# Optimization experiments

Hardware: AMD Instinct MI355X
Metric: run time of the kernel (lower is better)

The kernel has to match this reference:

```python
import jax, jax.numpy as jnp
import numpy as np

B, C, IN = 8, 1024, 256
OUT, H, NS, SD = 256, 4, 5, 64
DK = OUT // H


def setup_inputs() -> dict:
    key = jax.random.key(0)
    ks = jax.random.split(key, 16)
    s = lambda k, *shape: jax.random.normal(k, shape, dtype=jnp.float32) * 0.05
    return {
        "x": jax.random.normal(ks[0], (B, C, IN), dtype=jnp.float32),
        "A_prior": jax.random.uniform(ks[1], (C, C), dtype=jnp.float32),
        # lin_project
        "Wp": s(ks[2], IN, OUT), "bp": jnp.zeros((OUT,), jnp.float32),
        # stage_mlp: Linear(IN,128) -> ReLU -> Linear(128,NS)
        "Ws1": s(ks[3], IN, 128), "bs1": jnp.zeros((128,), jnp.float32),
        "Ws2": s(ks[4], 128, NS), "bs2": jnp.zeros((NS,), jnp.float32),
        # mlp_c: Linear(NS,SD) -> ReLU -> Linear(SD,SD)
        "Wc1": s(ks[5], NS, SD), "bc1": jnp.zeros((SD,), jnp.float32),
        "Wc2": s(ks[6], SD, SD), "bc2": jnp.zeros((SD,), jnp.float32),
        # att_scorer: Linear(2*DK+SD, 1, bias=False) -> weight vector
        "att_w": s(ks[7], 2 * DK + SD),
        "lam": jnp.ones((H,), jnp.float32),
    }


def reference(x, A_prior, Wp, bp, Ws1, bs1, Ws2, bs2, Wc1, bc1, Wc2, bc2, att_w, lam):
    # projection -> (B, C, H, DK)
    x_proj = (x @ Wp + bp).reshape(B, C, H, DK)
    # stage logits from mean-pooled features
    s_logits = jax.nn.relu(x.mean(axis=1) @ Ws1 + bs1) @ Ws2 + bs2  # (B, NS)
    s_prob = jax.nn.softmax(s_logits, axis=-1)
    c = jax.nn.relu(s_prob @ Wc1 + bc1) @ Wc2 + bc2  # (B, SD)
    # att_scorer is linear over cat([x_src, x_dst, c]); decompose weight to
    # avoid materializing the (B,C,C,H,2*DK+SD) concat tensor.
    w_src, w_dst, w_c = att_w[:DK], att_w[DK:2 * DK], att_w[2 * DK:]
    src_s = jnp.einsum('bjhd,d->bjh', x_proj, w_src)  # x_src[b,i,j] = x_proj[b,j]
    dst_s = jnp.einsum('bihd,d->bih', x_proj, w_dst)  # x_dst[b,i,j] = x_proj[b,i]
    c_s = c @ w_c                                      # (B,)
    e = jax.nn.leaky_relu(
        src_s[:, None, :, :] + dst_s[:, :, None, :] + c_s[:, None, None, None],
        negative_slope=0.2)                            # (B, C, C, H)
    prior = lam[None, None, None, :] * jnp.log(A_prior[None, :, :, None] + 1e-9)
    alpha = jax.nn.softmax(e + prior, axis=2)          # softmax over src j
    out = jnp.einsum('bijh,bjhd->bihd', alpha, x_proj).reshape(B, C, OUT)
    return out, s_logits
```

## Files before the change

### kernel.cpp

```cpp
#include <hip/hip_runtime.h>
#include <hip/hip_fp16.h>

typedef _Float16 f16x8 __attribute__((ext_vector_type(8)));
typedef _Float16 f16x4 __attribute__((ext_vector_type(4)));
typedef float f32x4 __attribute__((ext_vector_type(4)));

#define NB 8
#define NNS 5


__global__ __launch_bounds__(256) void k_pre(const float* __restrict__ Wp,
                                             const float* __restrict__ x,
                                             const float* __restrict__ A,
                                             __half* __restrict__ WpF,
                                             float* __restrict__ xmean,
                                             __half* __restrict__ l2AF) {
  const int t = threadIdx.x;
  const int blk = blockIdx.x;
  if (blk < 256) {
    const int idx = (blk << 8) + t;
    const int u = idx & 7, lane = (idx >> 3) & 63;
    const int kc = (idx >> 9) & 7, nt = (idx >> 12) & 3, nh = idx >> 14;
    const int f = (nh << 6) + (nt << 4) + (lane & 15);
    const int k = (kc << 5) + (((lane >> 4)) << 3) + u;
    WpF[idx] = __float2half(Wp[(k << 8) + f]);
  } else if (blk < 512) {
    const int row0 = (blk - 256) << 5;
    const int b = row0 >> 10;
    float ps = 0.f;
    #pragma unroll 8
    for (int r = 0; r < 32; ++r) ps += x[(size_t)(row0 + r) * 256 + t];
    atomicAdd(&xmean[(b << 8) + t], ps);
  } else {
    const int idx = ((blk - 512) << 8) + t;
    const int u = idx & 7, lane = (idx >> 3) & 63;
    const int jc = (idx >> 9) & 31, it = idx >> 14;
    const int row = (it << 4) + (lane & 15);
    const int j = (jc << 5) + ((lane >> 4) << 3) + u;
    l2AF[idx] = __float2half(__log2f(A[((size_t)row << 10) + j] + 1e-9f));
  }
}

__global__ __launch_bounds__(256, 4) void k_projM(
    const float* __restrict__ x, const __half* __restrict__ WpF,
    const float* __restrict__ bp, const float* __restrict__ att_w,
    __half* __restrict__ xpF, float* __restrict__ srcT,
    float* __restrict__ dstT) {
  __shared__ __align__(16) __half xs[64 * 256];
  const int t = threadIdx.x;
  const int l = t & 63, w = t >> 6;
  const int lm = l & 15, q = l >> 4;
  const int rg = blockIdx.x >> 2, nh = blockIdx.x & 3;
  const int row0 = rg << 6;

  #pragma unroll
  for (int it = 0; it < 16; ++it) {
    const int fi = (it << 8) + t;
    const int row = fi >> 6, c4 = fi & 63;
    const f32x4 v = *(const f32x4*)(x + (size_t)(row0 + row) * 256 + (c4 << 2));
    f16x4 hv;
    #pragma unroll
    for (int u = 0; u < 4; ++u) hv[u] = (_Float16)v[u];
    const int byte = (row << 9) + (c4 << 3);
    *(f16x4*)((char*)xs + (byte ^ ((row & 7) << 4))) = hv;
  }
  __syncthreads();

  const char* ar = (char*)xs + (((w << 4) + lm) << 9);
  const int xa = (lm & 7) << 4;
  const __half* Bw = WpF + (nh << 14) + (l << 3);

  f32x4 acc0 = {0.f, 0.f, 0.f, 0.f}, acc1 = acc0, acc2 = acc0, acc3 = acc0;
  #pragma unroll
  for (int kc = 0; kc < 8; ++kc) {
    const f16x8 af =
        *(const f16x8*)(ar + ((((kc << 5) + (q << 3)) << 1) ^ xa));
    const f16x8 b0 = *(const f16x8*)(Bw + (kc << 9));
    const f16x8 b1 = *(const f16x8*)(Bw + (kc << 9) + 4096);
    const f16x8 b2 = *(const f16x8*)(Bw + (kc << 9) + 8192);
    const f16x8 b3 = *(const f16x8*)(Bw + (kc << 9) + 12288);
    acc0 = __builtin_amdgcn_mfma_f32_16x16x32_f16(af, b0, acc0, 0, 0, 0);
    acc1 = __builtin_amdgcn_mfma_f32_16x16x32_f16(af, b1, acc1, 0, 0, 0);
    acc2 = __builtin_amdgcn_mfma_f32_16x16x32_f16(af, b2, acc2, 0, 0, 0);
    acc3 = __builtin_amdgcn_mfma_f32_16x16x32_f16(af, b3, acc3, 0, 0, 0);
  }

  const int Rw = row0 + (w << 4);
  const int b = Rw >> 10;
  const int il = (Rw & 1023) + (q << 2);
  const int jc = il >> 5, lq = (il >> 3) & 3, u0 = il & 7;
  const int lane_o = (lq << 4) + lm;
  f32x4 accs[4] = {acc0, acc1, acc2, acc3};
  float wsn[4], wdn[4];
  #pragma unroll
  for (int n = 0; n < 4; ++n) {
    const int d = (n << 4) + lm;
    wsn[n] = att_w[d];
    wdn[n] = att_w[64 + d];
  }
  const size_t base = ((((size_t)((b << 2) + nh) << 5) + jc) << 2);
  #pragma unroll
  for (int n = 0; n < 4; ++n) {
    const float bias = bp[(nh << 6) + (n << 4) + lm];
    f16x4 o;
    #pragma unroll
    for (int reg = 0; reg < 4; ++reg) {
      accs[n][reg] += bias;
      o[reg] = (_Float16)accs[n][reg];
    }
    *(f16x4*)(xpF + (((base + n) << 9) + (lane_o << 3) + u0)) = o;
  }
  #pragma unroll
  for (int reg = 0; reg < 4; ++reg) {
    float ss = 0.f, ds = 0.f;
    #pragma unroll
    for (int n = 0; n < 4; ++n) {
      ss = fmaf(accs[n][reg], wsn[n], ss);
      ds = fmaf(accs[n][reg], wdn[n], ds);
    }
    #pragma unroll
    for (int off = 1; off < 16; off <<= 1) {
      ss += __shfl_xor(ss, off);
      ds += __shfl_xor(ds, off);
    }
    if (lm == 0) {
      const int i = il + reg;
      srcT[(((b << 2) + nh) << 10) + i] = ss;
      dstT[(((b << 2) + nh) << 10) + i] = ds;
    }
  }
}

__global__ __launch_bounds__(256) void k_head(
    const float* __restrict__ Ws1, const float* __restrict__ bs1,
    const float* __restrict__ Ws2, const float* __restrict__ bs2,
    const float* __restrict__ Wc1, const float* __restrict__ bc1,
    const float* __restrict__ Wc2, const float* __restrict__ bc2,
    const float* __restrict__ att_w, const float* __restrict__ xmean,
    float* __restrict__ cs_ws, float* __restrict__ out_slogits) {
  __shared__ float xm[256];
  __shared__ float h1p[2][128];
  __shared__ float h1[128];
  __shared__ float sl[NNS];
  __shared__ float sp[NNS];
  __shared__ float cc1[64];
  __shared__ float cvec[64];
  const int b = blockIdx.x, t = threadIdx.x;
  xm[t] = xmean[b * 256 + t] * (1.f / 1024.f);
  __syncthreads();
  {
    const int kh = t >> 7, f = t & 127;
    const float* wcol = Ws1 + (kh << 7) * 128 + f;
    const float* xk = xm + (kh << 7);
    float a = 0.f;
    #pragma unroll 8
    for (int k = 0; k < 128; ++k) a = fmaf(xk[k], wcol[k * 128], a);
    h1p[kh][f] = a;
  }
  __syncthreads();
  if (t < 128) h1[t] = fmaxf(h1p[0][t] + h1p[1][t] + bs1[t], 0.f);
  __syncthreads();
  if (t < NNS) {
    float a = bs2[t];
    #pragma unroll 8
    for (int k = 0; k < 128; ++k) a = fmaf(h1[k], Ws2[k * NNS + t], a);
    sl[t] = a;
    out_slogits[b * NNS + t] = a;
  }
  __syncthreads();
  if (t == 0) {
    float m = sl[0];
    for (int n = 1; n < NNS; ++n) m = fmaxf(m, sl[n]);
    float s = 0.f;
    for (int n = 0; n < NNS; ++n) { sp[n] = expf(sl[n] - m); s += sp[n]; }
    for (int n = 0; n < NNS; ++n) sp[n] /= s;
  }
  __syncthreads();
  if (t < 64) {
    float a = bc1[t];
    #pragma unroll
    for (int n = 0; n < NNS; ++n) a = fmaf(sp[n], Wc1[n * 64 + t], a);
    cc1[t] = fmaxf(a, 0.f);
  }
  __syncthreads();
  if (t < 64) {
    float a = bc2[t];
    #pragma unroll 8
    for (int m = 0; m < 64; ++m) a = fmaf(cc1[m], Wc2[m * 64 + t], a);
    cvec[t] = a;
  }
  __syncthreads();
  if (t < 64) {
    float v = cvec[t] * att_w[128 + t];
    #pragma unroll
    for (int m = 32; m; m >>= 1) v += __shfl_xor(v, m);
    if (t == 0) cs_ws[b] = v;
  }
}

__global__ __launch_bounds__(1024, 8) void k_attn(
    const __half* __restrict__ xpF, const __half* __restrict__ l2AF,
    const float* __restrict__ srcT, const float* __restrict__ dstT,
    const float* __restrict__ cs_ws, const float* __restrict__ lam,
    float* __restrict__ out) {
  __shared__ float red[3][4][4][16][18];
  __shared__ float dsum[4][4][16];
  const int t = threadIdx.x;
  const int l = t & 63, w = t >> 6;
  const int h = w & 3, jq = w >> 2;
  const int lm = l & 15, q = l >> 4;
  const int b = blockIdx.x >> 6;
  const int tile = blockIdx.x & 63;
  const int i0 = tile << 4;

  const float csv = cs_ws[b];
  const float lamln2 = lam[h] * 0.69314718056f;
  const float dstc = dstT[(((b << 2) + h) << 10) + i0 + lm] + csv;

  const __half* Lp =
      l2AF + ((((size_t)(tile << 5) + (jq << 3)) << 6) + l) * 8;
  const float* Sp = srcT + (((b << 2) + h) << 10) + (jq << 8) + (q << 3);
  const __half* Bp =
      xpF + ((((size_t)((b << 2) + h) << 5) + (jq << 3)) << 11) + (l << 3);

  f32x4 acc0 = {0.f, 0.f, 0.f, 0.f}, acc1 = acc0, acc2 = acc0, acc3 = acc0;
  float sum = 0.f;

  #pragma unroll
  for (int kk = 0; kk < 8; ++kk) {
    const f16x8 la = *(const f16x8*)(Lp + (kk << 9));
    const f16x8 bf0 = *(const f16x8*)(Bp + (kk << 11));
    const f16x8 bf1 = *(const f16x8*)(Bp + (kk << 11) + 512);
    const f16x8 bf2 = *(const f16x8*)(Bp + (kk << 11) + 1024);
    const f16x8 bf3 = *(const f16x8*)(Bp + (kk << 11) + 1536);
    const f32x4 s0 = *(const f32x4*)(Sp + (kk << 5));
    const f32x4 s1 = *(const f32x4*)(Sp + (kk << 5) + 4);
    f16x8 af;
    #pragma unroll
    for (int u = 0; u < 4; ++u) {
      float e0 = s0[u] + dstc;
      e0 = fmaxf(e0, 0.2f * e0);
      const float p0 = __expf(fmaf(lamln2, (float)la[u], e0));
      sum += p0;
      af[u] = (_Float16)p0;
      float e1 = s1[u] + dstc;
      e1 = fmaxf(e1, 0.2f * e1);
      const float p1 = __expf(fmaf(lamln2, (float)la[u + 4], e1));
      sum += p1;
      af[u + 4] = (_Float16)p1;
    }
    acc0 = __builtin_amdgcn_mfma_f32_16x16x32_f16(af, bf0, acc0, 0, 0, 0);
    acc1 = __builtin_amdgcn_mfma_f32_16x16x32_f16(af, bf1, acc1, 0, 0, 0);
    acc2 = __builtin_amdgcn_mfma_f32_16x16x32_f16(af, bf2, acc2, 0, 0, 0);
    acc3 = __builtin_amdgcn_mfma_f32_16x16x32_f16(af, bf3, acc3, 0, 0, 0);
  }

  sum += __shfl_xor(sum, 16);
  sum += __shfl_xor(sum, 32);
  if (l < 16) dsum[h][jq][lm] = sum;
  if (jq != 0) {
    #pragma unroll
    for (int reg = 0; reg < 4; ++reg) {
      const int mrow = (q << 2) + reg;
      red[jq - 1][h][0][mrow][lm] = acc0[reg];
      red[jq - 1][h][1][mrow][lm] = acc1[reg];
      red[jq - 1][h][2][mrow][lm] = acc2[reg];
      red[jq - 1][h][3][mrow][lm] = acc3[reg];
    }
  }
  __syncthreads();
  if (jq == 0) {
    float* ob =
        out + (((size_t)((b << 10) + i0)) << 8) + (h << 6) + lm;
    #pragma unroll
    for (int reg = 0; reg < 4; ++reg) {
      const int mrow = (q << 2) + reg;
      const float dv = 1.f / (dsum[h][0][mrow] + dsum[h][1][mrow] +
                              dsum[h][2][mrow] + dsum[h][3][mrow]);
      const float v0 = acc0[reg] + red[0][h][0][mrow][lm] +
                       red[1][h][0][mrow][lm] + red[2][h][0][mrow][lm];
      const float v1 = acc1[reg] + red[0][h][1][mrow][lm] +
                       red[1][h][1][mrow][lm] + red[2][h][1][mrow][lm];
      const float v2 = acc2[reg] + red[0][h][2][mrow][lm] +
                       red[1][h][2][mrow][lm] + red[2][h][2][mrow][lm];
      const float v3 = acc3[reg] + red[0][h][3][mrow][lm] +
                       red[1][h][3][mrow][lm] + red[2][h][3][mrow][lm];
      float* orow = ob + ((size_t)mrow << 8);
      orow[0] = v0 * dv;
      orow[16] = v1 * dv;
      orow[32] = v2 * dv;
      orow[48] = v3 * dv;
    }
  }
}

extern "C" void kernel_launch(void* const* d_in, const int* in_sizes, int n_in,
                              void* d_out, int out_size, void* d_ws,
                              size_t ws_size, hipStream_t stream) {
  const float* x     = (const float*)d_in[0];
  const float* A     = (const float*)d_in[1];
  const float* Wp    = (const float*)d_in[2];
  const float* bp    = (const float*)d_in[3];
  const float* Ws1   = (const float*)d_in[4];
  const float* bs1   = (const float*)d_in[5];
  const float* Ws2   = (const float*)d_in[6];
  const float* bs2   = (const float*)d_in[7];
  const float* Wc1   = (const float*)d_in[8];
  const float* bc1   = (const float*)d_in[9];
  const float* Wc2   = (const float*)d_in[10];
  const float* bc2   = (const float*)d_in[11];
  const float* att_w = (const float*)d_in[12];
  const float* lam   = (const float*)d_in[13];
  float* out = (float*)d_out;
  float* ws  = (float*)d_ws;

  __half* xpF  = (__half*)ws;
  __half* l2AF = (__half*)(ws + 1048576);
  float* srcT  = ws + 1572864;
  float* dstT  = ws + 1605632;
  float* xmean = ws + 1638400;
  float* cs    = ws + 1640448;
  __half* WpF  = (__half*)(ws + 1640456);

  hipMemsetAsync(xmean, 0, 2048 * sizeof(float), stream);

  k_pre<<<dim3(4608), dim3(256), 0, stream>>>(Wp, x, A, WpF, xmean, l2AF);
  k_projM<<<dim3(512), dim3(256), 0, stream>>>(x, WpF, bp, att_w, xpF, srcT,
                                               dstT);
  k_head<<<dim3(NB), dim3(256), 0, stream>>>(Ws1, bs1, Ws2, bs2, Wc1, bc1,
                                             Wc2, bc2, att_w, xmean, cs,
                                             out + NB * 1024 * 256);
  k_attn<<<dim3(512), dim3(1024), 0, stream>>>(xpF, l2AF, srcT, dstT, cs, lam,
                                               out);
}
```

Measured before the change: 130.0 us.

## Fuse x fp16 conversion into pre-pass, halve attention split-K with prefetching

The mean-pooling pre-pass now also converts x to fp16 in MFMA-fragment order, so the projection kernel loads A-fragments straight from global memory without LDS staging. The attention kernel drops from 4 to 2 j-chunks per head (512 threads), with a 16-step loop that prefetches the next iteration's operands, which shrinks the cross-wave LDS reduction. Costs are an extra fp16 workspace buffer with its global write and read, and longer per-wave serial loops with higher register pressure.

```diff
diff --git a/kernel.cpp b/kernel.cpp
--- a/kernel.cpp
+++ b/kernel.cpp
@@ -14,7 +14,9 @@
                                              const float* __restrict__ A,
                                              __half* __restrict__ WpF,
                                              float* __restrict__ xmean,
+                                             __half* __restrict__ xF,
                                              __half* __restrict__ l2AF) {
+  __shared__ __align__(16) float xs[32][260];
   const int t = threadIdx.x;
   const int blk = blockIdx.x;
   if (blk < 256) {
@@ -22,15 +24,40 @@
     const int u = idx & 7, lane = (idx >> 3) & 63;
     const int kc = (idx >> 9) & 7, nt = (idx >> 12) & 3, nh = idx >> 14;
     const int f = (nh << 6) + (nt << 4) + (lane & 15);
-    const int k = (kc << 5) + (((lane >> 4)) << 3) + u;
+    const int k = (kc << 5) + ((lane >> 4) << 3) + u;
     WpF[idx] = __float2half(Wp[(k << 8) + f]);
   } else if (blk < 512) {
     const int row0 = (blk - 256) << 5;
     const int b = row0 >> 10;
+    const int rt0 = row0 >> 4;
     float ps = 0.f;
     #pragma unroll 8
-    for (int r = 0; r < 32; ++r) ps += x[(size_t)(row0 + r) * 256 + t];
+    for (int r = 0; r < 32; ++r) {
+      const float v = x[(size_t)(row0 + r) * 256 + t];
+      xs[r][t] = v;
+      ps += v;
+    }
     atomicAdd(&xmean[(b << 8) + t], ps);
+    __syncthreads();
+    #pragma unroll
+    for (int it = 0; it < 4; ++it) {
+      const int oi = it * 256 + t;
+      const int lane = oi & 63;
+      const int kc = (oi >> 6) & 7;
+      const int rtl = oi >> 9;
+      const int row_l = (rtl << 4) + (lane & 15);
+      const int k0 = (kc << 5) + ((lane >> 4) << 3);
+      const f32x4 va = *(const f32x4*)&xs[row_l][k0];
+      const f32x4 vb = *(const f32x4*)&xs[row_l][k0 + 4];
+      f16x8 hv;
+      #pragma unroll
+      for (int u = 0; u < 4; ++u) {
+        hv[u] = (_Float16)va[u];
+        hv[u + 4] = (_Float16)vb[u];
+      }
+      *(f16x8*)(xF + (((size_t)(rt0 + rtl)) << 12) + (kc << 9) + (lane << 3)) =
+          hv;
+    }
   } else {
     const int idx = ((blk - 512) << 8) + t;
     const int u = idx & 7, lane = (idx >> 3) & 63;
@@ -42,52 +69,39 @@
 }
 
 __global__ __launch_bounds__(256, 4) void k_projM(
-    const float* __restrict__ x, const __half* __restrict__ WpF,
+    const __half* __restrict__ xF, const __half* __restrict__ WpF,
     const float* __restrict__ bp, const float* __restrict__ att_w,
     __half* __restrict__ xpF, float* __restrict__ srcT,
     float* __restrict__ dstT) {
-  __shared__ __align__(16) __half xs[64 * 256];
   const int t = threadIdx.x;
   const int l = t & 63, w = t >> 6;
   const int lm = l & 15, q = l >> 4;
   const int rg = blockIdx.x >> 2, nh = blockIdx.x & 3;
-  const int row0 = rg << 6;
-
-  #pragma unroll
-  for (int it = 0; it < 16; ++it) {
-    const int fi = (it << 8) + t;
-    const int row = fi >> 6, c4 = fi & 63;
-    const f32x4 v = *(const f32x4*)(x + (size_t)(row0 + row) * 256 + (c4 << 2));
-    f16x4 hv;
-    #pragma unroll
-    for (int u = 0; u < 4; ++u) hv[u] = (_Float16)v[u];
-    const int byte = (row << 9) + (c4 << 3);
-    *(f16x4*)((char*)xs + (byte ^ ((row & 7) << 4))) = hv;
-  }
-  __syncthreads();
-
-  const char* ar = (char*)xs + (((w << 4) + lm) << 9);
-  const int xa = (lm & 7) << 4;
+  const int rt = (rg << 2) + w;
+  const int R0 = rt << 4;
+
+  const __half* Ap = xF + (((size_t)rt) << 12) + (l << 3);
   const __half* Bw = WpF + (nh << 14) + (l << 3);
 
+  f16x8 ah[8];
+  #pragma unroll
+  for (int kc = 0; kc < 8; ++kc) ah[kc] = *(const f16x8*)(Ap + (kc << 9));
+
   f32x4 acc0 = {0.f, 0.f, 0.f, 0.f}, acc1 = acc0, acc2 = acc0, acc3 = acc0;
   #pragma unroll
   for (int kc = 0; kc < 8; ++kc) {
-    const f16x8 af =
-        *(const f16x8*)(ar + ((((kc << 5) + (q << 3)) << 1) ^ xa));
     const f16x8 b0 = *(const f16x8*)(Bw + (kc << 9));
     const f16x8 b1 = *(const f16x8*)(Bw + (kc << 9) + 4096);
     const f16x8 b2 = *(const f16x8*)(Bw + (kc << 9) + 8192);
     const f16x8 b3 = *(const f16x8*)(Bw + (kc << 9) + 12288);
-    acc0 = __builtin_amdgcn_mfma_f32_16x16x32_f16(af, b0, acc0, 0, 0, 0);
-    acc1 = __builtin_amdgcn_mfma_f32_16x16x32_f16(af, b1, acc1, 0, 0, 0);
-    acc2 = __builtin_amdgcn_mfma_f32_16x16x32_f16(af, b2, acc2, 0, 0, 0);
-    acc3 = __builtin_amdgcn_mfma_f32_16x16x32_f16(af, b3, acc3, 0, 0, 0);
-  }
-
-  const int Rw = row0 + (w << 4);
-  const int b = Rw >> 10;
-  const int il = (Rw & 1023) + (q << 2);
+    acc0 = __builtin_amdgcn_mfma_f32_16x16x32_f16(ah[kc], b0, acc0, 0, 0, 0);
+    acc1 = __builtin_amdgcn_mfma_f32_16x16x32_f16(ah[kc], b1, acc1, 0, 0, 0);
+    acc2 = __builtin_amdgcn_mfma_f32_16x16x32_f16(ah[kc], b2, acc2, 0, 0, 0);
+    acc3 = __builtin_amdgcn_mfma_f32_16x16x32_f16(ah[kc], b3, acc3, 0, 0, 0);
+  }
+
+  const int b = R0 >> 10;
+  const int il = (R0 & 1023) + (q << 2);
   const int jc = il >> 5, lq = (il >> 3) & 3, u0 = il & 7;
   const int lane_o = (lq << 4) + lm;
   f32x4 accs[4] = {acc0, acc1, acc2, acc3};
@@ -198,16 +212,16 @@
   }
 }
 
-__global__ __launch_bounds__(1024, 8) void k_attn(
+__global__ __launch_bounds__(512, 4) void k_attn(
     const __half* __restrict__ xpF, const __half* __restrict__ l2AF,
     const float* __restrict__ srcT, const float* __restrict__ dstT,
     const float* __restrict__ cs_ws, const float* __restrict__ lam,
     float* __restrict__ out) {
-  __shared__ float red[3][4][4][16][18];
-  __shared__ float dsum[4][4][16];
+  __shared__ float red[4][4][16][18];
+  __shared__ float dsum[4][2][16];
   const int t = threadIdx.x;
   const int l = t & 63, w = t >> 6;
-  const int h = w & 3, jq = w >> 2;
+  const int h = w & 3, jh = w >> 2;
   const int lm = l & 15, q = l >> 4;
   const int b = blockIdx.x >> 6;
   const int tile = blockIdx.x & 63;
@@ -217,24 +231,33 @@
   const float lamln2 = lam[h] * 0.69314718056f;
   const float dstc = dstT[(((b << 2) + h) << 10) + i0 + lm] + csv;
 
-  const __half* Lp =
-      l2AF + ((((size_t)(tile << 5) + (jq << 3)) << 6) + l) * 8;
-  const float* Sp = srcT + (((b << 2) + h) << 10) + (jq << 8) + (q << 3);
+  const __half* Lp = l2AF + (tile << 14) + (jh << 13) + (l << 3);
+  const float* Sp = srcT + (((b << 2) + h) << 10) + (jh << 9) + (q << 3);
   const __half* Bp =
-      xpF + ((((size_t)((b << 2) + h) << 5) + (jq << 3)) << 11) + (l << 3);
+      xpF + (((size_t)((b << 2) + h)) << 16) + (jh << 15) + (l << 3);
 
   f32x4 acc0 = {0.f, 0.f, 0.f, 0.f}, acc1 = acc0, acc2 = acc0, acc3 = acc0;
   float sum = 0.f;
 
-  #pragma unroll
-  for (int kk = 0; kk < 8; ++kk) {
-    const f16x8 la = *(const f16x8*)(Lp + (kk << 9));
-    const f16x8 bf0 = *(const f16x8*)(Bp + (kk << 11));
-    const f16x8 bf1 = *(const f16x8*)(Bp + (kk << 11) + 512);
-    const f16x8 bf2 = *(const f16x8*)(Bp + (kk << 11) + 1024);
-    const f16x8 bf3 = *(const f16x8*)(Bp + (kk << 11) + 1536);
-    const f32x4 s0 = *(const f32x4*)(Sp + (kk << 5));
-    const f32x4 s1 = *(const f32x4*)(Sp + (kk << 5) + 4);
+  f16x8 la = *(const f16x8*)Lp;
+  f32x4 s0 = *(const f32x4*)Sp;
+  f32x4 s1 = *(const f32x4*)(Sp + 4);
+  f16x8 bf0 = *(const f16x8*)Bp;
+  f16x8 bf1 = *(const f16x8*)(Bp + 512);
+  f16x8 bf2 = *(const f16x8*)(Bp + 1024);
+  f16x8 bf3 = *(const f16x8*)(Bp + 1536);
+
+  #pragma unroll 4
+  for (int kk = 0; kk < 16; ++kk) {
+    const int nk = (kk < 15) ? kk + 1 : kk;
+    const f16x8 la_n = *(const f16x8*)(Lp + (nk << 9));
+    const f32x4 s0_n = *(const f32x4*)(Sp + (nk << 5));
+    const f32x4 s1_n = *(const f32x4*)(Sp + (nk << 5) + 4);
+    const f16x8 b0_n = *(const f16x8*)(Bp + (nk << 11));
+    const f16x8 b1_n = *(const f16x8*)(Bp + (nk << 11) + 512);
+    const f16x8 b2_n = *(const f16x8*)(Bp + (nk << 11) + 1024);
+    const f16x8 b3_n = *(const f16x8*)(Bp + (nk << 11) + 1536);
+
     f16x8 af;
     #pragma unroll
     for (int u = 0; u < 4; ++u) {
@@ -253,43 +276,35 @@
     acc1 = __builtin_amdgcn_mfma_f32_16x16x32_f16(af, bf1, acc1, 0, 0, 0);
     acc2 = __builtin_amdgcn_mfma_f32_16x16x32_f16(af, bf2, acc2, 0, 0, 0);
     acc3 = __builtin_amdgcn_mfma_f32_16x16x32_f16(af, bf3, acc3, 0, 0, 0);
+    la = la_n; s0 = s0_n; s1 = s1_n;
+    bf0 = b0_n; bf1 = b1_n; bf2 = b2_n; bf3 = b3_n;
   }
 
   sum += __shfl_xor(sum, 16);
   sum += __shfl_xor(sum, 32);
-  if (l < 16) dsum[h][jq][lm] = sum;
-  if (jq != 0) {
+  if (l < 16) dsum[h][jh][lm] = sum;
+  if (jh == 1) {
     #pragma unroll
     for (int reg = 0; reg < 4; ++reg) {
       const int mrow = (q << 2) + reg;
-      red[jq - 1][h][0][mrow][lm] = acc0[reg];
-      red[jq - 1][h][1][mrow][lm] = acc1[reg];
-      red[jq - 1][h][2][mrow][lm] = acc2[reg];
-      red[jq - 1][h][3][mrow][lm] = acc3[reg];
-    }
-  }
-  __syncthreads();
-  if (jq == 0) {
-    float* ob =
-        out + (((size_t)((b << 10) + i0)) << 8) + (h << 6) + lm;
+      red[h][0][mrow][lm] = acc0[reg];
+      red[h][1][mrow][lm] = acc1[reg];
+      red[h][2][mrow][lm] = acc2[reg];
+      red[h][3][mrow][lm] = acc3[reg];
+    }
+  }
+  __syncthreads();
+  if (jh == 0) {
+    float* ob = out + (((size_t)((b << 10) + i0)) << 8) + (h << 6) + lm;
     #pragma unroll
     for (int reg = 0; reg < 4; ++reg) {
       const int mrow = (q << 2) + reg;
-      const float dv = 1.f / (dsum[h][0][mrow] + dsum[h][1][mrow] +
-                              dsum[h][2][mrow] + dsum[h][3][mrow]);
-      const float v0 = acc0[reg] + red[0][h][0][mrow][lm] +
-                       red[1][h][0][mrow][lm] + red[2][h][0][mrow][lm];
-      const float v1 = acc1[reg] + red[0][h][1][mrow][lm] +
-                       red[1][h][1][mrow][lm] + red[2][h][1][mrow][lm];
-      const float v2 = acc2[reg] + red[0][h][2][mrow][lm] +
-                       red[1][h][2][mrow][lm] + red[2][h][2][mrow][lm];
-      const float v3 = acc3[reg] + red[0][h][3][mrow][lm] +
-                       red[1][h][3][mrow][lm] + red[2][h][3][mrow][lm];
+      const float dv = 1.f / (dsum[h][0][mrow] + dsum[h][1][mrow]);
       float* orow = ob + ((size_t)mrow << 8);
-      orow[0] = v0 * dv;
-      orow[16] = v1 * dv;
-      orow[32] = v2 * dv;
-      orow[48] = v3 * dv;
+      orow[0] = (acc0[reg] + red[h][0][mrow][lm]) * dv;
+      orow[16] = (acc1[reg] + red[h][1][mrow][lm]) * dv;
+      orow[32] = (acc2[reg] + red[h][2][mrow][lm]) * dv;
+      orow[48] = (acc3[reg] + red[h][3][mrow][lm]) * dv;
     }
   }
 }
@@ -316,20 +331,21 @@
 
   __half* xpF  = (__half*)ws;
   __half* l2AF = (__half*)(ws + 1048576);
-  float* srcT  = ws + 1572864;
-  float* dstT  = ws + 1605632;
-  float* xmean = ws + 1638400;
-  float* cs    = ws + 1640448;
-  __half* WpF  = (__half*)(ws + 1640456);
+  __half* xF   = (__half*)(ws + 1572864);
+  float* srcT  = ws + 2621440;
+  float* dstT  = ws + 2654208;
+  float* xmean = ws + 2686976;
+  float* cs    = ws + 2689024;
+  __half* WpF  = (__half*)(ws + 2689032);
 
   hipMemsetAsync(xmean, 0, 2048 * sizeof(float), stream);
 
-  k_pre<<<dim3(4608), dim3(256), 0, stream>>>(Wp, x, A, WpF, xmean, l2AF);
-  k_projM<<<dim3(512), dim3(256), 0, stream>>>(x, WpF, bp, att_w, xpF, srcT,
+  k_pre<<<dim3(4608), dim3(256), 0, stream>>>(Wp, x, A, WpF, xmean, xF, l2AF);
+  k_projM<<<dim3(512), dim3(256), 0, stream>>>(xF, WpF, bp, att_w, xpF, srcT,
                                                dstT);
   k_head<<<dim3(NB), dim3(256), 0, stream>>>(Ws1, bs1, Ws2, bs2, Wc1, bc1,
                                              Wc2, bc2, att_w, xmean, cs,
                                              out + NB * 1024 * 256);
-  k_attn<<<dim3(512), dim3(1024), 0, stream>>>(xpF, l2AF, srcT, dstT, cs, lam,
-                                               out);
-}
+  k_attn<<<dim3(512), dim3(512), 0, stream>>>(xpF, l2AF, srcT, dstT, cs, lam,
+                                              out);
+}
```

Measured after the change: 129.0 us. Within noise of the previous version (-0.8%).
